# Optimization experiments

Hardware: AMD Instinct MI355X
Metric: run time of the kernel (lower is better)

## Reference

```python
import jax, jax.numpy as jnp
import numpy as np

N = 50000      # nodes
E = 800000     # edges (before self-loops)
IN = 256       # in_channels
HID = 16       # hidden_channels per head
HEADS = 8
OUT = 64       # out_channels (classes)
NEG_SLOPE = 0.2  # PyG GATConv leaky_relu slope


def setup_inputs() -> dict:
    key = jax.random.key(0)
    ks = jax.random.split(key, 10)
    x = jax.random.normal(ks[0], (N, IN), jnp.float32)
    edge_index = jax.random.randint(ks[1], (2, E), 0, N, dtype=jnp.int32)
    g = lambda k, shape: jax.random.normal(k, shape, jnp.float32) * (1.0 / np.sqrt(shape[0]))
    W1 = g(ks[2], (IN, HEADS * HID))
    a_src1 = jax.random.normal(ks[3], (HEADS, HID), jnp.float32) * 0.1
    a_dst1 = jax.random.normal(ks[4], (HEADS, HID), jnp.float32) * 0.1
    b1 = jnp.zeros((HEADS * HID,), jnp.float32)
    W2 = g(ks[5], (HEADS * HID, OUT))
    a_src2 = jax.random.normal(ks[6], (1, OUT), jnp.float32) * 0.1
    a_dst2 = jax.random.normal(ks[7], (1, OUT), jnp.float32) * 0.1
    b2 = jnp.zeros((OUT,), jnp.float32)
    return {"x": x, "edge_index": edge_index, "W1": W1, "a_src1": a_src1,
            "a_dst1": a_dst1, "b1": b1, "W2": W2, "a_src2": a_src2,
            "a_dst2": a_dst2, "b2": b2}


def gat_conv(x, src, dst, W, a_s, a_d, b, heads, concat):
    # x: [n, f]; edges src->dst; attention softmax over incoming edges of dst
    n = x.shape[0]
    h = (x @ W).reshape(n, heads, -1)                 # [n, H, d]
    al_s = jnp.einsum('nhd,hd->nh', h, a_s)           # [n, H]
    al_d = jnp.einsum('nhd,hd->nh', h, a_d)
    e = jax.nn.leaky_relu(al_s[src] + al_d[dst], negative_slope=NEG_SLOPE)  # [E, H]
    m = jax.ops.segment_max(e, dst, num_segments=n)   # stable scatter-softmax
    ex = jnp.exp(e - m[dst])
    den = jax.ops.segment_sum(ex, dst, num_segments=n)
    alpha = ex / (den[dst] + 1e-16)                   # [E, H]
    out = jax.ops.segment_sum(h[src] * alpha[:, :, None], dst, num_segments=n)  # [n, H, d]
    out = out.reshape(n, -1) if concat else out.mean(axis=1)
    return out + b


def reference(x, edge_index, W1, a_src1, a_dst1, b1, W2, a_src2, a_dst2, b2):
    # inference mode: dropout disabled. PyG GATConv adds self-loops by default.
    n = x.shape[0]
    loop = jnp.arange(n, dtype=edge_index.dtype)
    ei = jnp.concatenate([edge_index, jnp.stack([loop, loop])], axis=1)
    src, dst = ei[0], ei[1]
    h = gat_conv(x, src, dst, W1, a_src1, a_dst1, b1, HEADS, True)
    h = jax.nn.elu(h)
    h = gat_conv(h, src, dst, W2, a_src2, a_dst2, b2, 1, False)
    return jax.nn.log_softmax(h, axis=1)
```

## Files before the change

### kernel.cpp

```cpp
#include <hip/hip_runtime.h>
#include <hip/hip_bf16.h>


typedef __attribute__((ext_vector_type(8))) short short8;
typedef __attribute__((ext_vector_type(4))) float f4;
typedef __attribute__((ext_vector_type(2))) float float2v;

#define NCHUNK 64
#define NRANGE 4
#define RSIZE 16384
#define G1PAD 136
#define G2PAD 136

__device__ __forceinline__ unsigned short f2bf(float f) {
  unsigned int u = __builtin_bit_cast(unsigned int, f);
  u += 0x7fffu + ((u >> 16) & 1u);
  return (unsigned short)(u >> 16);
}
__device__ __forceinline__ float bf2f(unsigned short h) {
  unsigned int u = ((unsigned int)h) << 16;
  return __builtin_bit_cast(float, u);
}

__device__ __forceinline__ unsigned char f2fp8(float f) {
  unsigned int u = __builtin_bit_cast(unsigned int, f);
  unsigned int s = (u >> 24) & 0x80u;
  float a = fabsf(f);
  a = fminf(a, 448.f);
  if (a < 0.015625f) {
    int m = (int)rintf(a * 512.f);
    return (unsigned char)(s | (unsigned)m);
  }
  unsigned int ub = __builtin_bit_cast(unsigned int, a);
  ub += 0xFFFFFu + ((ub >> 20) & 1u);
  unsigned int e = (ub >> 23) - 120u;
  unsigned int m = (ub >> 20) & 7u;
  if (e > 15u) { e = 15u; m = 6u; }
  return (unsigned char)(s | (e << 3) | m);
}

__global__ __launch_bounds__(512) void hist_kernel(const int* __restrict__ ei,
                                                   int* __restrict__ hist,
                                                   int E, int N, int ET, int CS) {
  __shared__ int lh[RSIZE];
  const int c = blockIdx.x & (NCHUNK - 1);
  const int r = blockIdx.x >> 6;
  const int base = r * RSIZE;
  for (int i = threadIdx.x; i < RSIZE; i += 512) lh[i] = 0;
  __syncthreads();
  const int e0 = c * CS, e1 = min(e0 + CS, ET);
  for (int e = e0 + threadIdx.x; e < e1; e += 512) {
    int d = (e < E) ? ei[E + e] : (e - E);
    unsigned dl = (unsigned)(d - base);
    if (dl < RSIZE) atomicAdd(&lh[dl], 1);
  }
  __syncthreads();
  for (int i = threadIdx.x; i < RSIZE; i += 512) {
    int d = base + i;
    if (d < N) hist[c * N + d] = lh[i];
  }
}

__global__ __launch_bounds__(256) void colscan_kernel(int* __restrict__ hist,
                                                      int* __restrict__ deg, int N) {
  int d = blockIdx.x * 256 + threadIdx.x;
  if (d >= N) return;
  int run = 0;
#pragma unroll 8
  for (int c = 0; c < NCHUNK; ++c) {
    int v = hist[c * N + d];
    hist[c * N + d] = run;
    run += v;
  }
  deg[d] = run;
}

__global__ __launch_bounds__(1024) void scan1_kernel(const int* __restrict__ deg,
                                                     int* __restrict__ rowptr,
                                                     int* __restrict__ bsum, int N) {
  __shared__ int wtot[16];
  const int lane = threadIdx.x & 63, wid = threadIdx.x >> 6;
  int i = blockIdx.x * 1024 + threadIdx.x;
  int v = (i < N) ? deg[i] : 0;
  int incl = v;
#pragma unroll
  for (int off = 1; off < 64; off <<= 1) {
    int t = __shfl_up(incl, off, 64);
    if (lane >= off) incl += t;
  }
  if (lane == 63) wtot[wid] = incl;
  __syncthreads();
  int woff = 0;
#pragma unroll
  for (int w = 0; w < 16; ++w) woff += (w < wid) ? wtot[w] : 0;
  if (i < N) rowptr[i] = woff + incl - v;
  if (threadIdx.x == 1023) bsum[blockIdx.x] = woff + incl;
}

__global__ __launch_bounds__(64) void scan2_kernel(int* __restrict__ bsum, int NB) {
  int lane = threadIdx.x;
  int v = (lane < NB) ? bsum[lane] : 0;
  int incl = v;
#pragma unroll
  for (int off = 1; off < 64; off <<= 1) {
    int t = __shfl_up(incl, off, 64);
    if (lane >= off) incl += t;
  }
  if (lane < NB) bsum[lane] = incl - v;
}

__global__ __launch_bounds__(256) void scan3_kernel(int* __restrict__ rowptr,
                                                    const int* __restrict__ bsum,
                                                    int N, int ET) {
  int i = blockIdx.x * 256 + threadIdx.x;
  if (i < N) rowptr[i] += bsum[i >> 10];
  if (i == N) rowptr[N] = ET;
}

__global__ __launch_bounds__(512) void scatter2_kernel(const int* __restrict__ ei,
                                                       const int* __restrict__ hist,
                                                       const int* __restrict__ rowptr,
                                                       int* __restrict__ csr_src,
                                                       int E, int N, int ET, int CS) {
  __shared__ int lh[RSIZE];
  const int c = blockIdx.x & (NCHUNK - 1);
  const int r = blockIdx.x >> 6;
  const int base = r * RSIZE;
  for (int i = threadIdx.x; i < RSIZE; i += 512) {
    int d = base + i;
    lh[i] = (d < N) ? (rowptr[d] + hist[c * N + d]) : 0;
  }
  __syncthreads();
  const int e0 = c * CS, e1 = min(e0 + CS, ET);
  for (int e = e0 + threadIdx.x; e < e1; e += 512) {
    int s, d;
    if (e < E) { s = ei[e]; d = ei[E + e]; }
    else       { s = e - E; d = s; }
    unsigned dl = (unsigned)(d - base);
    if (dl < RSIZE) {
      int slot = atomicAdd(&lh[dl], 1);
      csr_src[slot] = s;
    }
  }
}

__global__ __launch_bounds__(256) void convw_kernel(const float* __restrict__ W1,
                                                    const float* __restrict__ W2,
                                                    unsigned short* __restrict__ Wt1,
                                                    unsigned short* __restrict__ Wt2) {
  int i = blockIdx.x * blockDim.x + threadIdx.x;
  if (i < 128 * 256) {
    int n = i >> 8, k = i & 255;
    Wt1[i] = f2bf(W1[k * 128 + n]);
  } else {
    int j = i - 128 * 256;
    if (j < 64 * 128) {
      int n = j >> 7, k = j & 127;
      Wt2[j] = f2bf(W2[k * 64 + n]);
    }
  }
}

__global__ __launch_bounds__(256, 3) void gemm1_mfma(const float* __restrict__ X,
                                                     const unsigned short* __restrict__ Wt,
                                                     unsigned char* __restrict__ H,
                                                     int M) {
  __shared__ unsigned short bl[128 * G1PAD];
  const int t = threadIdx.x;
  const int wv = t >> 6, ln = t & 63;
  const int ml = ln & 15, q = ln >> 4;
  const int r0 = blockIdx.x * 64 + wv * 16;
  const int arow = min(r0 + ml, M - 1);
  const float* xp = X + (size_t)arow * 256 + q * 8;

  float4 a0[8], a1[8];
#pragma unroll
  for (int s = 0; s < 8; ++s) {
    a0[s] = *(const float4*)(xp + s * 32);
    a1[s] = *(const float4*)(xp + s * 32 + 4);
  }

  f4 acc[8];
#pragma unroll
  for (int b = 0; b < 8; ++b) acc[b] = (f4)0.f;

  const int crow = t >> 1, coff = (t & 1) * 64;
#pragma unroll
  for (int half = 0; half < 2; ++half) {
    __syncthreads();
    {
      const unsigned short* src = Wt + (size_t)crow * 256 + half * 128 + coff;
      unsigned short* dst = &bl[crow * G1PAD + coff];
#pragma unroll
      for (int c = 0; c < 8; ++c)
        *(short8*)(dst + c * 8) = *(const short8*)(src + c * 8);
    }
    __syncthreads();
#pragma unroll
    for (int sl = 0; sl < 4; ++sl) {
      const int s = half * 4 + sl;
      short8 av;
      av[0] = (short)f2bf(a0[s].x); av[1] = (short)f2bf(a0[s].y);
      av[2] = (short)f2bf(a0[s].z); av[3] = (short)f2bf(a0[s].w);
      av[4] = (short)f2bf(a1[s].x); av[5] = (short)f2bf(a1[s].y);
      av[6] = (short)f2bf(a1[s].z); av[7] = (short)f2bf(a1[s].w);
#pragma unroll
      for (int b = 0; b < 8; ++b) {
        short8 bfr = *(const short8*)&bl[(b * 16 + ml) * G1PAD + sl * 32 + q * 8];
        acc[b] = __builtin_amdgcn_mfma_f32_16x16x32_bf16(av, bfr, acc[b], 0, 0, 0);
      }
    }
  }

#pragma unroll
  for (int i = 0; i < 4; ++i) {
    int rr = r0 + q * 4 + i;
    if (rr < M) {
#pragma unroll
      for (int b = 0; b < 8; ++b)
        H[(size_t)rr * 128 + b * 16 + ml] = f2fp8(acc[b][i]);
    }
  }
}

__global__ __launch_bounds__(256, 4) void gemm2_mfma(const unsigned short* __restrict__ Xb,
                                                     const unsigned short* __restrict__ Wt,
                                                     unsigned char* __restrict__ H,
                                                     int M) {
  __shared__ unsigned short bl[64 * G2PAD];
  const int t = threadIdx.x;
  const int wv = t >> 6, ln = t & 63;
  const int ml = ln & 15, q = ln >> 4;
  const int r0 = blockIdx.x * 64 + wv * 16;
  const int arow = min(r0 + ml, M - 1);
  const unsigned short* xp = Xb + (size_t)arow * 128 + q * 8;

  short8 av[4];
#pragma unroll
  for (int s = 0; s < 4; ++s) av[s] = *(const short8*)(xp + s * 32);

  {
    const int crow = t >> 2, coff = (t & 3) * 32;
    const unsigned short* src = Wt + (size_t)crow * 128 + coff;
    unsigned short* dst = &bl[crow * G2PAD + coff];
#pragma unroll
    for (int c = 0; c < 4; ++c)
      *(short8*)(dst + c * 8) = *(const short8*)(src + c * 8);
  }
  __syncthreads();

  f4 acc[4];
#pragma unroll
  for (int b = 0; b < 4; ++b) acc[b] = (f4)0.f;

#pragma unroll
  for (int s = 0; s < 4; ++s) {
#pragma unroll
    for (int b = 0; b < 4; ++b) {
      short8 bfr = *(const short8*)&bl[(b * 16 + ml) * G2PAD + s * 32 + q * 8];
      acc[b] = __builtin_amdgcn_mfma_f32_16x16x32_bf16(av[s], bfr, acc[b], 0, 0, 0);
    }
  }

#pragma unroll
  for (int i = 0; i < 4; ++i) {
    int rr = r0 + q * 4 + i;
    if (rr < M) {
#pragma unroll
      for (int b = 0; b < 4; ++b)
        H[(size_t)rr * 64 + b * 16 + ml] = f2fp8(acc[b][i]);
    }
  }
}

__global__ __launch_bounds__(256) void dots1_kernel(const unsigned char* __restrict__ h1,
                                                    const float* __restrict__ as,
                                                    const float* __restrict__ ad,
                                                    float* __restrict__ als,
                                                    float* __restrict__ ald, int N) {
  int wave = (blockIdx.x * blockDim.x + threadIdx.x) >> 6;
  int lane = threadIdx.x & 63;
  if (wave >= N) return;
  unsigned short pk = *(const unsigned short*)(h1 + (size_t)wave * 128 + 2 * lane);
  float2v g = __builtin_amdgcn_cvt_pk_f32_fp8(pk, false);
  float s = g.x * as[2 * lane] + g.y * as[2 * lane + 1];
  float d = g.x * ad[2 * lane] + g.y * ad[2 * lane + 1];
#pragma unroll
  for (int off = 1; off < 8; off <<= 1) {
    s += __shfl_xor(s, off, 8);
    d += __shfl_xor(d, off, 8);
  }
  if ((lane & 7) == 0) {
    int h = lane >> 3;
    als[wave * 8 + h] = s;
    ald[wave * 8 + h] = d;
  }
}

__global__ __launch_bounds__(256) void dots2_kernel(const unsigned char* __restrict__ h2,
                                                    const float* __restrict__ as,
                                                    const float* __restrict__ ad,
                                                    float* __restrict__ als,
                                                    float* __restrict__ ald, int N) {
  int wave = (blockIdx.x * blockDim.x + threadIdx.x) >> 6;
  int lane = threadIdx.x & 63;
  if (wave >= N) return;
  float x = __builtin_amdgcn_cvt_f32_fp8(h2[(size_t)wave * 64 + lane], 0);
  float s = x * as[lane], d = x * ad[lane];
#pragma unroll
  for (int off = 32; off; off >>= 1) {
    s += __shfl_xor(s, off, 64);
    d += __shfl_xor(d, off, 64);
  }
  if (lane == 0) { als[wave] = s; ald[wave] = d; }
}

__global__ __launch_bounds__(256) void attn1_kernel(
    const unsigned char* __restrict__ h1, const float* __restrict__ als,
    const float* __restrict__ ald, const float* __restrict__ b1,
    const int* __restrict__ rowptr, const int* __restrict__ csr_src,
    unsigned short* __restrict__ helu, int N) {
  int d = __builtin_amdgcn_readfirstlane(
      (blockIdx.x * blockDim.x + threadIdx.x) >> 6);
  int lane = threadIdx.x & 63;
  if (d >= N) return;
  const int hh = lane >> 3;
  const int hw = lane & 7;
  const int ew = lane >> 3;
  const float aldp = ald[d * 8 + hw];
  const int beg = rowptr[d], end = rowptr[d + 1];
  const unsigned char* h1l = h1 + 2 * lane;
  float den = 0.f, ax = 0.f, ay = 0.f;

  for (int p0 = beg; p0 < end; p0 += 8) {
    int idx = p0 + ew;
    int se = csr_src[idx < end ? idx : end - 1];
    float v = als[se * 8 + hw] + aldp;
    v = fmaxf(v, 0.2f * v);
    float w = (idx < end) ? __expf(v) : 0.f;
#pragma unroll
    for (int j = 0; j < 4; ++j) {
      float wj = __shfl(w, j * 8 + hh);
      int sj = __shfl(se, j * 8);
      unsigned short pk = *(const unsigned short*)(h1l + (size_t)sj * 128);
      float2v g = __builtin_amdgcn_cvt_pk_f32_fp8(pk, false);
      den += wj; ax += wj * g.x; ay += wj * g.y;
    }
    if (p0 + 4 < end) {
#pragma unroll
      for (int j = 4; j < 8; ++j) {
        float wj = __shfl(w, j * 8 + hh);
        int sj = __shfl(se, j * 8);
        unsigned short pk = *(const unsigned short*)(h1l + (size_t)sj * 128);
        float2v g = __builtin_amdgcn_cvt_pk_f32_fp8(pk, false);
        den += wj; ax += wj * g.x; ay += wj * g.y;
      }
    }
  }

  float inv = 1.0f / (den + 1e-16f);
  float2 bb = *(const float2*)(b1 + 2 * lane);
  float o0 = ax * inv + bb.x;
  float o1 = ay * inv + bb.y;
  o0 = o0 > 0.f ? o0 : __expf(o0) - 1.0f;
  o1 = o1 > 0.f ? o1 : __expf(o1) - 1.0f;
  ushort2 ov; ov.x = f2bf(o0); ov.y = f2bf(o1);
  *(ushort2*)(helu + (size_t)d * 128 + 2 * lane) = ov;
}

__global__ __launch_bounds__(256) void attn2_kernel(
    const unsigned char* __restrict__ h2, const float* __restrict__ als,
    const float* __restrict__ ald, const float* __restrict__ b2,
    const int* __restrict__ rowptr, const int* __restrict__ csr_src,
    float* __restrict__ out, int N) {
  int d = __builtin_amdgcn_readfirstlane(
      (blockIdx.x * blockDim.x + threadIdx.x) >> 6);
  int lane = threadIdx.x & 63;
  if (d >= N) return;
  const float aldd = ald[d];
  const int beg = rowptr[d], end = rowptr[d + 1];
  const unsigned char* h2l = h2 + lane;
  float den = 0.f, acc = 0.f;

  for (int p0 = beg; p0 < end; p0 += 64) {
    int idx = p0 + lane;
    int se = csr_src[idx < end ? idx : end - 1];
    float v = als[se] + aldd;
    v = fmaxf(v, 0.2f * v);
    float w = (idx < end) ? __expf(v) : 0.f;
    int cnt = min(64, end - p0);
    for (int j0 = 0; j0 < cnt; j0 += 4) {
#pragma unroll
      for (int j = 0; j < 4; ++j) {
        float wj = __shfl(w, j0 + j);
        int sj = __shfl(se, j0 + j);
        float g = __builtin_amdgcn_cvt_f32_fp8(h2l[(size_t)sj * 64], 0);
        den += wj; acc += wj * g;
      }
    }
  }

  float z = acc / (den + 1e-16f) + b2[lane];
  float zm = z;
#pragma unroll
  for (int off = 32; off; off >>= 1) zm = fmaxf(zm, __shfl_xor(zm, off, 64));
  float ex = __expf(z - zm), se2 = ex;
#pragma unroll
  for (int off = 32; off; off >>= 1) se2 += __shfl_xor(se2, off, 64);
  out[(size_t)d * 64 + lane] = z - zm - __logf(se2);
}

extern "C" void kernel_launch(void* const* d_in, const int* in_sizes, int n_in,
                              void* d_out, int out_size, void* d_ws, size_t ws_size,
                              hipStream_t stream) {
  const int N = in_sizes[0] / 256;
  const int E = in_sizes[1] / 2;
  const int ET = E + N;
  const int CS = (ET + NCHUNK - 1) / NCHUNK;
  const int NB = (N + 1023) / 1024;

  const float* x   = (const float*)d_in[0];
  const int*   ei  = (const int*)d_in[1];
  const float* W1  = (const float*)d_in[2];
  const float* as1 = (const float*)d_in[3];
  const float* ad1 = (const float*)d_in[4];
  const float* b1  = (const float*)d_in[5];
  const float* W2  = (const float*)d_in[6];
  const float* as2 = (const float*)d_in[7];
  const float* ad2 = (const float*)d_in[8];
  const float* b2  = (const float*)d_in[9];
  float* out = (float*)d_out;

  char* p = (char*)d_ws;
  unsigned char* h1f8 = (unsigned char*)p; p += (size_t)N * 128;
  unsigned char* h2f8 = h1f8;
  unsigned short* helu = (unsigned short*)p; p += (size_t)NCHUNK * N * 4;
  int* hist = (int*)helu;
  unsigned short* Wt1  = (unsigned short*)p; p += (size_t)128 * 256 * 2;
  unsigned short* Wt2  = (unsigned short*)p; p += (size_t)64 * 128 * 2;
  float* als1 = (float*)p; p += (size_t)N * 8 * 4;
  float* ald1 = (float*)p; p += (size_t)N * 8 * 4;
  float* als2 = (float*)p; p += (size_t)N * 4;
  float* ald2 = (float*)p; p += (size_t)N * 4;
  int* deg     = (int*)p; p += (size_t)N * 4;
  int* rowptr  = (int*)p; p += (size_t)(N + 1) * 4;
  int* bsum    = (int*)p; p += 64 * 4;
  int* csr_src = (int*)p; p += (size_t)ET * 4;

  convw_kernel<<<(128 * 256 + 64 * 128 + 255) / 256, 256, 0, stream>>>(W1, W2, Wt1, Wt2);

  hist_kernel<<<NCHUNK * NRANGE, 512, 0, stream>>>(ei, hist, E, N, ET, CS);
  colscan_kernel<<<(N + 255) / 256, 256, 0, stream>>>(hist, deg, N);
  scan1_kernel<<<NB, 1024, 0, stream>>>(deg, rowptr, bsum, N);
  scan2_kernel<<<1, 64, 0, stream>>>(bsum, NB);
  scan3_kernel<<<(N + 256) / 256, 256, 0, stream>>>(rowptr, bsum, N, ET);
  scatter2_kernel<<<NCHUNK * NRANGE, 512, 0, stream>>>(ei, hist, rowptr, csr_src, E, N, ET, CS);

  gemm1_mfma<<<(N + 63) / 64, 256, 0, stream>>>(x, Wt1, h1f8, N);
  dots1_kernel<<<(N + 3) / 4, 256, 0, stream>>>(h1f8, as1, ad1, als1, ald1, N);
  attn1_kernel<<<(N + 3) / 4, 256, 0, stream>>>(h1f8, als1, ald1, b1, rowptr, csr_src, helu, N);

  gemm2_mfma<<<(N + 63) / 64, 256, 0, stream>>>(helu, Wt2, h2f8, N);
  dots2_kernel<<<(N + 3) / 4, 256, 0, stream>>>(h2f8, as2, ad2, als2, ald2, N);
  attn2_kernel<<<(N + 3) / 4, 256, 0, stream>>>(h2f8, als2, ald2, b2, rowptr, csr_src, out, N);
}
```

Before: 266.2 us.

## Fuse attention dot products into GEMM epilogues and merge small setup kernels

```diff
diff --git a/kernel.cpp b/kernel.cpp
--- a/kernel.cpp
+++ b/kernel.cpp
@@ -11,6 +11,7 @@
 #define RSIZE 16384
 #define G1PAD 136
 #define G2PAD 136
+#define CONVB 80
 
 __device__ __forceinline__ unsigned short f2bf(float f) {
   unsigned int u = __builtin_bit_cast(unsigned int, f);
@@ -41,7 +42,25 @@
 
 __global__ __launch_bounds__(512) void hist_kernel(const int* __restrict__ ei,
                                                    int* __restrict__ hist,
+                                                   const float* __restrict__ W1,
+                                                   const float* __restrict__ W2,
+                                                   unsigned short* __restrict__ Wt1,
+                                                   unsigned short* __restrict__ Wt2,
                                                    int E, int N, int ET, int CS) {
+  if (blockIdx.x >= NCHUNK * NRANGE) {
+    int i = (blockIdx.x - NCHUNK * NRANGE) * 512 + threadIdx.x;
+    if (i < 128 * 256) {
+      int n = i >> 8, k = i & 255;
+      Wt1[i] = f2bf(W1[k * 128 + n]);
+    } else {
+      int j = i - 128 * 256;
+      if (j < 64 * 128) {
+        int n = j >> 7, k = j & 127;
+        Wt2[j] = f2bf(W2[k * 64 + n]);
+      }
+    }
+    return;
+  }
   __shared__ int lh[RSIZE];
   const int c = blockIdx.x & (NCHUNK - 1);
   const int r = blockIdx.x >> 6;
@@ -97,23 +116,16 @@
   if (threadIdx.x == 1023) bsum[blockIdx.x] = woff + incl;
 }
 
-__global__ __launch_bounds__(64) void scan2_kernel(int* __restrict__ bsum, int NB) {
-  int lane = threadIdx.x;
-  int v = (lane < NB) ? bsum[lane] : 0;
-  int incl = v;
-#pragma unroll
-  for (int off = 1; off < 64; off <<= 1) {
-    int t = __shfl_up(incl, off, 64);
-    if (lane >= off) incl += t;
-  }
-  if (lane < NB) bsum[lane] = incl - v;
-}
-
 __global__ __launch_bounds__(256) void scan3_kernel(int* __restrict__ rowptr,
                                                     const int* __restrict__ bsum,
                                                     int N, int ET) {
+  int lane = threadIdx.x & 63;
+  int g = blockIdx.x >> 2;
+  int bv = (lane < g) ? bsum[lane] : 0;
+#pragma unroll
+  for (int off = 32; off; off >>= 1) bv += __shfl_xor(bv, off, 64);
   int i = blockIdx.x * 256 + threadIdx.x;
-  if (i < N) rowptr[i] += bsum[i >> 10];
+  if (i < N) rowptr[i] += bv;
   if (i == N) rowptr[N] = ET;
 }
 
@@ -144,26 +156,13 @@
   }
 }
 
-__global__ __launch_bounds__(256) void convw_kernel(const float* __restrict__ W1,
-                                                    const float* __restrict__ W2,
-                                                    unsigned short* __restrict__ Wt1,
-                                                    unsigned short* __restrict__ Wt2) {
-  int i = blockIdx.x * blockDim.x + threadIdx.x;
-  if (i < 128 * 256) {
-    int n = i >> 8, k = i & 255;
-    Wt1[i] = f2bf(W1[k * 128 + n]);
-  } else {
-    int j = i - 128 * 256;
-    if (j < 64 * 128) {
-      int n = j >> 7, k = j & 127;
-      Wt2[j] = f2bf(W2[k * 64 + n]);
-    }
-  }
-}
-
 __global__ __launch_bounds__(256, 3) void gemm1_mfma(const float* __restrict__ X,
                                                      const unsigned short* __restrict__ Wt,
+                                                     const float* __restrict__ as1,
+                                                     const float* __restrict__ ad1,
                                                      unsigned char* __restrict__ H,
+                                                     float* __restrict__ als,
+                                                     float* __restrict__ ald,
                                                      int M) {
   __shared__ unsigned short bl[128 * G1PAD];
   const int t = threadIdx.x;
@@ -215,17 +214,36 @@
 #pragma unroll
   for (int i = 0; i < 4; ++i) {
     int rr = r0 + q * 4 + i;
-    if (rr < M) {
+    bool ok = rr < M;
+    if (ok) {
 #pragma unroll
       for (int b = 0; b < 8; ++b)
         H[(size_t)rr * 128 + b * 16 + ml] = f2fp8(acc[b][i]);
     }
+#pragma unroll
+    for (int b = 0; b < 8; ++b) {
+      float ps = acc[b][i] * as1[b * 16 + ml];
+      float pd = acc[b][i] * ad1[b * 16 + ml];
+#pragma unroll
+      for (int off = 1; off < 16; off <<= 1) {
+        ps += __shfl_xor(ps, off, 16);
+        pd += __shfl_xor(pd, off, 16);
+      }
+      if (ok && ml == b) {
+        als[(size_t)rr * 8 + b] = ps;
+        ald[(size_t)rr * 8 + b] = pd;
+      }
+    }
   }
 }
 
 __global__ __launch_bounds__(256, 4) void gemm2_mfma(const unsigned short* __restrict__ Xb,
                                                      const unsigned short* __restrict__ Wt,
+                                                     const float* __restrict__ as2,
+                                                     const float* __restrict__ ad2,
                                                      unsigned char* __restrict__ H,
+                                                     float* __restrict__ als,
+                                                     float* __restrict__ ald,
                                                      int M) {
   __shared__ unsigned short bl[64 * G2PAD];
   const int t = threadIdx.x;
@@ -265,54 +283,25 @@
 #pragma unroll
   for (int i = 0; i < 4; ++i) {
     int rr = r0 + q * 4 + i;
-    if (rr < M) {
+    bool ok = rr < M;
+    if (ok) {
 #pragma unroll
       for (int b = 0; b < 4; ++b)
         H[(size_t)rr * 64 + b * 16 + ml] = f2fp8(acc[b][i]);
     }
-  }
-}
-
-__global__ __launch_bounds__(256) void dots1_kernel(const unsigned char* __restrict__ h1,
-                                                    const float* __restrict__ as,
-                                                    const float* __restrict__ ad,
-                                                    float* __restrict__ als,
-                                                    float* __restrict__ ald, int N) {
-  int wave = (blockIdx.x * blockDim.x + threadIdx.x) >> 6;
-  int lane = threadIdx.x & 63;
-  if (wave >= N) return;
-  unsigned short pk = *(const unsigned short*)(h1 + (size_t)wave * 128 + 2 * lane);
-  float2v g = __builtin_amdgcn_cvt_pk_f32_fp8(pk, false);
-  float s = g.x * as[2 * lane] + g.y * as[2 * lane + 1];
-  float d = g.x * ad[2 * lane] + g.y * ad[2 * lane + 1];
-#pragma unroll
-  for (int off = 1; off < 8; off <<= 1) {
-    s += __shfl_xor(s, off, 8);
-    d += __shfl_xor(d, off, 8);
-  }
-  if ((lane & 7) == 0) {
-    int h = lane >> 3;
-    als[wave * 8 + h] = s;
-    ald[wave * 8 + h] = d;
-  }
-}
-
-__global__ __launch_bounds__(256) void dots2_kernel(const unsigned char* __restrict__ h2,
-                                                    const float* __restrict__ as,
-                                                    const float* __restrict__ ad,
-                                                    float* __restrict__ als,
-                                                    float* __restrict__ ald, int N) {
-  int wave = (blockIdx.x * blockDim.x + threadIdx.x) >> 6;
-  int lane = threadIdx.x & 63;
-  if (wave >= N) return;
-  float x = __builtin_amdgcn_cvt_f32_fp8(h2[(size_t)wave * 64 + lane], 0);
-  float s = x * as[lane], d = x * ad[lane];
-#pragma unroll
-  for (int off = 32; off; off >>= 1) {
-    s += __shfl_xor(s, off, 64);
-    d += __shfl_xor(d, off, 64);
-  }
-  if (lane == 0) { als[wave] = s; ald[wave] = d; }
+    float ps = 0.f, pd = 0.f;
+#pragma unroll
+    for (int b = 0; b < 4; ++b) {
+      ps += acc[b][i] * as2[b * 16 + ml];
+      pd += acc[b][i] * ad2[b * 16 + ml];
+    }
+#pragma unroll
+    for (int off = 1; off < 16; off <<= 1) {
+      ps += __shfl_xor(ps, off, 16);
+      pd += __shfl_xor(pd, off, 16);
+    }
+    if (ok && ml == 0) { als[rr] = ps; ald[rr] = pd; }
+  }
 }
 
 __global__ __launch_bounds__(256) void attn1_kernel(
@@ -447,20 +436,16 @@
   int* bsum    = (int*)p; p += 64 * 4;
   int* csr_src = (int*)p; p += (size_t)ET * 4;
 
-  convw_kernel<<<(128 * 256 + 64 * 128 + 255) / 256, 256, 0, stream>>>(W1, W2, Wt1, Wt2);
-
-  hist_kernel<<<NCHUNK * NRANGE, 512, 0, stream>>>(ei, hist, E, N, ET, CS);
+  hist_kernel<<<NCHUNK * NRANGE + CONVB, 512, 0, stream>>>(ei, hist, W1, W2, Wt1, Wt2,
+                                                           E, N, ET, CS);
   colscan_kernel<<<(N + 255) / 256, 256, 0, stream>>>(hist, deg, N);
   scan1_kernel<<<NB, 1024, 0, stream>>>(deg, rowptr, bsum, N);
-  scan2_kernel<<<1, 64, 0, stream>>>(bsum, NB);
   scan3_kernel<<<(N + 256) / 256, 256, 0, stream>>>(rowptr, bsum, N, ET);
   scatter2_kernel<<<NCHUNK * NRANGE, 512, 0, stream>>>(ei, hist, rowptr, csr_src, E, N, ET, CS);
 
-  gemm1_mfma<<<(N + 63) / 64, 256, 0, stream>>>(x, Wt1, h1f8, N);
-  dots1_kernel<<<(N + 3) / 4, 256, 0, stream>>>(h1f8, as1, ad1, als1, ald1, N);
+  gemm1_mfma<<<(N + 63) / 64, 256, 0, stream>>>(x, Wt1, as1, ad1, h1f8, als1, ald1, N);
   attn1_kernel<<<(N + 3) / 4, 256, 0, stream>>>(h1f8, als1, ald1, b1, rowptr, csr_src, helu, N);
 
-  gemm2_mfma<<<(N + 63) / 64, 256, 0, stream>>>(helu, Wt2, h2f8, N);
-  dots2_kernel<<<(N + 3) / 4, 256, 0, stream>>>(h2f8, as2, ad2, als2, ald2, N);
+  gemm2_mfma<<<(N + 63) / 64, 256, 0, stream>>>(helu, Wt2, as2, ad2, h2f8, als2, ald2, N);
   attn2_kernel<<<(N + 3) / 4, 256, 0, stream>>>(h2f8, als2, ald2, b2, rowptr, csr_src, out, N);
 }
```

Measured after the change: 253.8 us. -4.7%, faster.
